# Kernel tuning notes

Measured on AMD Instinct MI355X. Metric: run time of the kernel, lower is better.

The kernel has to match this reference:

```python
import jax, jax.numpy as jnp
import numpy as np

B, A, T, D, H, NB, OUT = 64, 128, 6, 256, 512, 5, 401
ALPHA = 0.5
BETA = 0.5


def _lin_init(key, n_in, n_out, extra=()):
    bound = 1.0 / np.sqrt(n_in)
    kw, kb = jax.random.split(key)
    W = jax.random.uniform(kw, extra + (n_in, n_out), minval=-bound, maxval=bound, dtype=jnp.float32)
    b = jax.random.uniform(kb, extra + (n_out,), minval=-bound, maxval=bound, dtype=jnp.float32)
    return W, b


def setup_inputs() -> dict:
    key = jax.random.key(0)
    ks = jax.random.split(key, 8)
    stdv = 1.0 / np.sqrt(D)
    anchor = jax.random.uniform(ks[0], (1, 1, T, D), minval=-stdv, maxval=stdv, dtype=jnp.float32)
    sW1, sb1 = _lin_init(ks[1], D, D, (NB,))
    sW2, sb2 = _lin_init(ks[2], D, D, (NB,))
    cW1, cb1 = _lin_init(ks[3], D, D, (NB,))
    cW2, cb2 = _lin_init(ks[4], D, D, (NB,))
    dW1, db1 = _lin_init(ks[5], D, H)
    dW2, db2 = _lin_init(ks[6], H, OUT)
    final_embedding = jax.random.normal(ks[7], (B, A, D), dtype=jnp.float32)
    return {"final_embedding": final_embedding, "anchor": anchor,
            "sW1": sW1, "sb1": sb1, "sW2": sW2, "sb2": sb2,
            "cW1": cW1, "cb1": cb1, "cW2": cW2, "cb2": cb2,
            "dW1": dW1, "db1": db1, "dW2": dW2, "db2": db2}


def _mlp2(x, W1, b1, W2, b2):
    # 2-layer MLP (Linear -> ReLU -> Linear), applied to last dim
    return jax.nn.relu(x @ W1 + b1) @ W2 + b2


def reference(final_embedding, anchor, sW1, sb1, sW2, sb2, cW1, cb1, cW2, cb2, dW1, db1, dW2, db2):
    b, a = final_embedding.shape[:2]
    # s: [B, A, T, D] repeated anchors; c: [B, A, 1, D] context
    s = jnp.broadcast_to(anchor, (b, a, T, D))
    c = final_embedding[:, :, None, :]
    for i in range(NB):
        s_new = _mlp2(s, sW1[i], sb1[i], sW2[i], sb2[i])
        c_new = _mlp2(c, cW1[i], cb1[i], cW2[i], cb2[i])
        s_new = s_new * c_new                      # gate, broadcasts over T
        agg_c = jnp.max(s_new, axis=-2, keepdims=True)
        s = ALPHA * s + BETA * s_new               # sliding running mean
        c = ALPHA * c + BETA * agg_c
    # decoder MLP on trajectory embeddings s: [B, A, T, D]
    res = jax.nn.relu(s @ dW1 + db1) @ dW2 + db2   # [B, A, T, 401]
    coordinates = res[..., :160].reshape(b, a, T, 80, 2)
    av = res[..., 160:240].reshape(b, a, T, 80, 1)
    bv = res[..., 240:320].reshape(b, a, T, 80, 1)
    cv = res[..., 320:400].reshape(b, a, T, 80, 1)
    probas = res[..., -1]                          # [B, A, T]
    cov = jnp.concatenate([jnp.exp(av) * jnp.cosh(bv), jnp.sinh(bv),
                           jnp.sinh(bv), jnp.exp(-av) * jnp.cosh(bv)], axis=-1) * jnp.exp(cv)
    covariance_matrices = cov.reshape(b, a, T, 80, 2, 2)
    return (probas, coordinates, covariance_matrices)
```

## Files before the change

kernel.cpp:

```cpp
#include <hip/hip_runtime.h>
#include <math.h>


constexpr int Tn  = 6;
constexpr int Dn  = 256;
constexpr int Hn  = 512;
constexpr int NBn = 5;
constexpr int OUTn = 401;
constexpr int BA  = 8192;
constexpr int MR  = 49152;
constexpr float kAlpha = 0.5f;
constexpr float kBeta  = 0.5f;

typedef __bf16 bf16_8 __attribute__((ext_vector_type(8)));
typedef float  f32x4  __attribute__((ext_vector_type(4)));

__device__ __forceinline__ void async_copy16(const __bf16* g, __bf16* l) {
  __builtin_amdgcn_global_load_lds(
      (const __attribute__((address_space(1))) void*)g,
      (__attribute__((address_space(3))) void*)l, 16, 0, 0);
}

template<bool RELU, bool OUT_BF16>
__global__ __launch_bounds__(256) void gemm_mfma(
    const __bf16* __restrict__ A, const __bf16* __restrict__ BT,
    const float* __restrict__ bias, void* __restrict__ Cout,
    int M, int N, int K)
{
  __shared__ __align__(16) char smem[34816];

  const int tid = threadIdx.x;
  const int l   = tid & 63;
  const int w   = tid >> 6;
  const int wm  = w >> 1, wn = w & 1;

  const int GX = gridDim.x;
  const int total = GX * gridDim.y;
  const int L = blockIdx.y * GX + blockIdx.x;
  const int xcd = L & 7, pos = L >> 3;
  const int base = total >> 3, rem = total & 7;
  const int start = xcd * base + (xcd < rem ? xcd : rem);
  const int TL = start + pos;
  const int my = TL / GX;
  const int nx = TL - my * GX;
  const int m0 = my * 128;
  const int n0 = nx * 128;

  const int lrow = l >> 2;
  const int lk   = (l & 3) * 8;
  int ar0 = m0 + w * 32 + lrow;        if (ar0 > M - 1) ar0 = M - 1;
  int ar1 = m0 + w * 32 + 16 + lrow;   if (ar1 > M - 1) ar1 = M - 1;
  int br0 = n0 + w * 32 + lrow;        if (br0 > N - 1) br0 = N - 1;
  int br1 = n0 + w * 32 + 16 + lrow;   if (br1 > N - 1) br1 = N - 1;
  const __bf16* Ag0 = A  + (size_t)ar0 * K + lk;
  const __bf16* Ag1 = A  + (size_t)ar1 * K + lk;
  const __bf16* Bg0 = BT + (size_t)br0 * K + lk;
  const __bf16* Bg1 = BT + (size_t)br1 * K + lk;

  f32x4 acc[4][4];
#pragma unroll
  for (int i = 0; i < 4; ++i)
#pragma unroll
    for (int j = 0; j < 4; ++j) acc[i][j] = (f32x4){0.f, 0.f, 0.f, 0.f};

  auto stage = [&](int buf, int ko) {
    __bf16* As = (__bf16*)(smem + buf * 16384);
    __bf16* Bs = As + 4096;
    async_copy16(Ag0 + ko, As + w * 1024);
    async_copy16(Ag1 + ko, As + w * 1024 + 512);
    async_copy16(Bg0 + ko, Bs + w * 1024);
    async_copy16(Bg1 + ko, Bs + w * 1024 + 512);
  };

  const int kIters = K >> 5;
  stage(0, 0);
  __syncthreads();
  for (int kt = 0; kt < kIters; ++kt) {
    if (kt + 1 < kIters) stage((kt + 1) & 1, (kt + 1) * 32);
    const __bf16* As = (const __bf16*)(smem + (kt & 1) * 16384);
    const __bf16* Bs = As + 4096;
    const __bf16* ap = As + (wm * 64 + (l & 15)) * 32 + (l >> 4) * 8;
    const __bf16* bp = Bs + (wn * 64 + (l & 15)) * 32 + (l >> 4) * 8;

    bf16_8 af[4], bf[4];
#pragma unroll
    for (int i = 0; i < 4; ++i) af[i] = *(const bf16_8*)(ap + i * 16 * 32);
#pragma unroll
    for (int j = 0; j < 4; ++j) bf[j] = *(const bf16_8*)(bp + j * 16 * 32);
#pragma unroll
    for (int i = 0; i < 4; ++i)
#pragma unroll
      for (int j = 0; j < 4; ++j)
        acc[i][j] = __builtin_amdgcn_mfma_f32_16x16x32_bf16(af[i], bf[j], acc[i][j], 0, 0, 0);
    __syncthreads();
  }

  const int colb = n0 + wn * 64 + (l & 15);
  const int rowb = m0 + wm * 64 + (l >> 4) * 4;

  if (OUT_BF16) {
    __bf16* Cs = (__bf16*)smem;
    const int lrb = wm * 64 + (l >> 4) * 4;
    const int lcb = wn * 64 + (l & 15);
#pragma unroll
    for (int j = 0; j < 4; ++j) {
      const float bj = bias[colb + j * 16];
#pragma unroll
      for (int i = 0; i < 4; ++i) {
#pragma unroll
        for (int r = 0; r < 4; ++r) {
          float v = acc[i][j][r] + bj;
          if (RELU) v = fmaxf(v, 0.0f);
          Cs[(lrb + i * 16 + r) * 136 + lcb + j * 16] = (__bf16)v;
        }
      }
    }
    __syncthreads();
    __bf16* Cg = (__bf16*)Cout;
#pragma unroll
    for (int it = 0; it < 8; ++it) {
      const int idx = it * 256 + tid;
      const int row = idx >> 4, c16 = idx & 15;
      const int gr = m0 + row;
      if (gr < M) {
        uint4 v = *(const uint4*)(Cs + row * 136 + c16 * 8);
        *(uint4*)(Cg + (size_t)gr * N + n0 + c16 * 8) = v;
      }
    }
  } else {
#pragma unroll
    for (int j = 0; j < 4; ++j) {
      const int gc = colb + j * 16;
      if (gc >= N) continue;
      const float bj = bias[gc];
#pragma unroll
      for (int i = 0; i < 4; ++i) {
        const int gr0 = rowb + i * 16;
#pragma unroll
        for (int r = 0; r < 4; ++r) {
          const int gr = gr0 + r;
          if (gr >= M) continue;
          float v = acc[i][j][r] + bj;
          if (RELU) v = fmaxf(v, 0.0f);
          ((float*)Cout)[(size_t)gr * N + gc] = v;
        }
      }
    }
  }
}

__global__ __launch_bounds__(512) void mlp2_c(
    const __bf16* __restrict__ X, const __bf16* __restrict__ W1T,
    const float* __restrict__ b1, const __bf16* __restrict__ W2T,
    const float* __restrict__ b2, __bf16* __restrict__ Out)
{
  __shared__ __align__(16) char smem[53248];
  __bf16* Hb = (__bf16*)(smem + 36864);

  const int tid = threadIdx.x, l = tid & 63, w = tid >> 6;
  const int m0 = blockIdx.x * 32;
  const int q4 = (l >> 4) * 4;

  f32x4 acc[2][2];
#pragma unroll
  for (int i = 0; i < 2; ++i)
#pragma unroll
    for (int j = 0; j < 2; ++j) acc[i][j] = (f32x4){0.f, 0.f, 0.f, 0.f};

  const __bf16* Xg = X + (size_t)(m0 + (tid >> 2)) * Dn + (tid & 3) * 8;

  auto stageA = [&](int buf, int kt) {
    if (tid < 128)
      async_copy16(Xg + kt * 32, (__bf16*)(smem + buf * 2048) + tid * 8);
  };
  auto stageW = [&](const __bf16* WT, int buf, int kt) {
    __bf16* Wstb = (__bf16*)(smem + 4096 + buf * 16384);
#pragma unroll
    for (int r2 = 0; r2 < 2; ++r2) {
      const int ch = tid + r2 * 512, row = ch >> 2, kk = (ch & 3) * 8;
      async_copy16(WT + (size_t)row * Dn + kt * 32 + kk, Wstb + ch * 8);
    }
  };

  stageA(0, 0); stageW(W1T, 0, 0);
  __syncthreads();
  for (int kt = 0; kt < 8; ++kt) {
    if (kt < 7) { stageA((kt + 1) & 1, kt + 1); stageW(W1T, (kt + 1) & 1, kt + 1); }
    const __bf16* Astb = (const __bf16*)(smem + (kt & 1) * 2048);
    const __bf16* Wstb = (const __bf16*)(smem + 4096 + (kt & 1) * 16384);
    bf16_8 bf[2];
#pragma unroll
    for (int j = 0; j < 2; ++j)
      bf[j] = *(const bf16_8*)(Wstb + (w * 32 + j * 16 + (l & 15)) * 32 + (l >> 4) * 8);
#pragma unroll
    for (int i = 0; i < 2; ++i) {
      bf16_8 af = *(const bf16_8*)(Astb + (i * 16 + (l & 15)) * 32 + (l >> 4) * 8);
#pragma unroll
      for (int j = 0; j < 2; ++j)
        acc[i][j] = __builtin_amdgcn_mfma_f32_16x16x32_bf16(af, bf[j], acc[i][j], 0, 0, 0);
    }
    __syncthreads();
  }

#pragma unroll
  for (int j = 0; j < 2; ++j) {
    const int col = w * 32 + j * 16 + (l & 15);
    const float bj = b1[col];
    __bf16* hc = Hb + (col >> 5) * 1024 + (col & 31);
#pragma unroll
    for (int i = 0; i < 2; ++i)
#pragma unroll
      for (int r = 0; r < 4; ++r) {
        const int row = i * 16 + q4 + r;
        hc[row * 32] = (__bf16)fmaxf(acc[i][j][r] + bj, 0.0f);
      }
  }
  __syncthreads();

#pragma unroll
  for (int i = 0; i < 2; ++i)
#pragma unroll
    for (int j = 0; j < 2; ++j) acc[i][j] = (f32x4){0.f, 0.f, 0.f, 0.f};
  stageW(W2T, 0, 0);
  __syncthreads();
  for (int kt = 0; kt < 8; ++kt) {
    if (kt < 7) stageW(W2T, (kt + 1) & 1, kt + 1);
    const __bf16* Wstb = (const __bf16*)(smem + 4096 + (kt & 1) * 16384);
    bf16_8 bf[2];
#pragma unroll
    for (int j = 0; j < 2; ++j)
      bf[j] = *(const bf16_8*)(Wstb + (w * 32 + j * 16 + (l & 15)) * 32 + (l >> 4) * 8);
#pragma unroll
    for (int i = 0; i < 2; ++i) {
      bf16_8 af = *(const bf16_8*)(Hb + kt * 1024 + (i * 16 + (l & 15)) * 32 + (l >> 4) * 8);
#pragma unroll
      for (int j = 0; j < 2; ++j)
        acc[i][j] = __builtin_amdgcn_mfma_f32_16x16x32_bf16(af, bf[j], acc[i][j], 0, 0, 0);
    }
    __syncthreads();
  }

#pragma unroll
  for (int j = 0; j < 2; ++j) {
    const int col = w * 32 + j * 16 + (l & 15);
    const float bj = b2[col];
#pragma unroll
    for (int i = 0; i < 2; ++i)
#pragma unroll
      for (int r = 0; r < 4; ++r) {
        const int row = i * 16 + q4 + r;
        Out[(size_t)(m0 + row) * Dn + col] = (__bf16)(acc[i][j][r] + bj);
      }
  }
}

__global__ __launch_bounds__(512) void mlp2_cs(
    __bf16* __restrict__ S,
    const __bf16* __restrict__ sW1T, const float* __restrict__ sb1,
    const __bf16* __restrict__ sW2T, const float* __restrict__ sb2,
    const __bf16* __restrict__ cW1T, const float* __restrict__ cb1,
    const __bf16* __restrict__ cW2T, const float* __restrict__ cb2,
    __bf16* __restrict__ C)
{
  __shared__ __align__(16) char smem[71680];
  __bf16* Hb    = (__bf16*)(smem + 22528);
  __bf16* Snew  = (__bf16*)smem;
  __bf16* Hc    = (__bf16*)(smem + 45056);
  __bf16* CnewL = (__bf16*)(smem + 53248);

  const int tid = threadIdx.x, l = tid & 63, w = tid >> 6;
  const int m0  = blockIdx.x * 96;
  const int ba0 = blockIdx.x * 16;
  const int q4  = (l >> 4) * 4;

  {
    f32x4 ac[2];
    ac[0] = (f32x4){0.f, 0.f, 0.f, 0.f};
    ac[1] = (f32x4){0.f, 0.f, 0.f, 0.f};

    const __bf16* Cg = C + (size_t)(ba0 + (tid >> 2)) * Dn + (tid & 3) * 8;

    auto stageC1 = [&](int buf, int kt) {
      __bf16* Astb = (__bf16*)(smem + buf * 22528);
      __bf16* Wstb = Astb + 3072;
      if (tid < 64) async_copy16(Cg + kt * 32, Astb + tid * 8);
#pragma unroll
      for (int r2 = 0; r2 < 2; ++r2) {
        const int ch = tid + r2 * 512, row = ch >> 2, kk = (ch & 3) * 8;
        async_copy16(cW1T + (size_t)row * Dn + kt * 32 + kk, Wstb + ch * 8);
      }
    };
    stageC1(0, 0);
    __syncthreads();
    for (int kt = 0; kt < 8; ++kt) {
      if (kt < 7) stageC1((kt + 1) & 1, kt + 1);
      const __bf16* Astb = (const __bf16*)(smem + (kt & 1) * 22528);
      const __bf16* Wstb = Astb + 3072;
      bf16_8 bf[2];
#pragma unroll
      for (int j = 0; j < 2; ++j)
        bf[j] = *(const bf16_8*)(Wstb + (w * 32 + j * 16 + (l & 15)) * 32 + (l >> 4) * 8);
      bf16_8 af = *(const bf16_8*)(Astb + (l & 15) * 32 + (l >> 4) * 8);
#pragma unroll
      for (int j = 0; j < 2; ++j)
        ac[j] = __builtin_amdgcn_mfma_f32_16x16x32_bf16(af, bf[j], ac[j], 0, 0, 0);
      __syncthreads();
    }

#pragma unroll
    for (int j = 0; j < 2; ++j) {
      const int col = w * 32 + j * 16 + (l & 15);
      const float bj = cb1[col];
      __bf16* hc = Hc + (col >> 5) * 512 + (col & 31);
#pragma unroll
      for (int r = 0; r < 4; ++r)
        hc[(q4 + r) * 32] = (__bf16)fmaxf(ac[j][r] + bj, 0.0f);
    }
    __syncthreads();

    ac[0] = (f32x4){0.f, 0.f, 0.f, 0.f};
    ac[1] = (f32x4){0.f, 0.f, 0.f, 0.f};
    auto stageC2 = [&](int buf, int kt) {
      __bf16* Wstb = (__bf16*)(smem + buf * 22528 + 6144);
#pragma unroll
      for (int r2 = 0; r2 < 2; ++r2) {
        const int ch = tid + r2 * 512, row = ch >> 2, kk = (ch & 3) * 8;
        async_copy16(cW2T + (size_t)row * Dn + kt * 32 + kk, Wstb + ch * 8);
      }
    };
    stageC2(0, 0);
    __syncthreads();
    for (int kt = 0; kt < 8; ++kt) {
      if (kt < 7) stageC2((kt + 1) & 1, kt + 1);
      const __bf16* Wstb = (const __bf16*)(smem + (kt & 1) * 22528 + 6144);
      bf16_8 bf[2];
#pragma unroll
      for (int j = 0; j < 2; ++j)
        bf[j] = *(const bf16_8*)(Wstb + (w * 32 + j * 16 + (l & 15)) * 32 + (l >> 4) * 8);
      bf16_8 af = *(const bf16_8*)(Hc + kt * 512 + (l & 15) * 32 + (l >> 4) * 8);
#pragma unroll
      for (int j = 0; j < 2; ++j)
        ac[j] = __builtin_amdgcn_mfma_f32_16x16x32_bf16(af, bf[j], ac[j], 0, 0, 0);
      __syncthreads();
    }

#pragma unroll
    for (int j = 0; j < 2; ++j) {
      const int col = w * 32 + j * 16 + (l & 15);
      const float bj = cb2[col];
#pragma unroll
      for (int r = 0; r < 4; ++r)
        CnewL[(q4 + r) * 264 + col] = (__bf16)(ac[j][r] + bj);
    }
    __syncthreads();
  }

  bf16_8 cn8 = *(const bf16_8*)(CnewL + (tid >> 5) * 264 + (tid & 31) * 8);

  f32x4 acc[6][2];
#pragma unroll
  for (int i = 0; i < 6; ++i)
#pragma unroll
    for (int j = 0; j < 2; ++j) acc[i][j] = (f32x4){0.f, 0.f, 0.f, 0.f};

  const __bf16* Sg = S + (size_t)(m0 + (tid >> 2)) * Dn + (tid & 3) * 8;

  auto stageL1 = [&](int buf, int kt) {
    __bf16* Astb = (__bf16*)(smem + buf * 22528);
    __bf16* Wstb = (__bf16*)(smem + buf * 22528 + 6144);
    if (tid < 384) async_copy16(Sg + kt * 32, Astb + tid * 8);
#pragma unroll
    for (int r2 = 0; r2 < 2; ++r2) {
      const int ch = tid + r2 * 512, row = ch >> 2, kk = (ch & 3) * 8;
      async_copy16(sW1T + (size_t)row * Dn + kt * 32 + kk, Wstb + ch * 8);
    }
  };

  stageL1(0, 0);
  __syncthreads();
  for (int kt = 0; kt < 8; ++kt) {
    if (kt < 7) stageL1((kt + 1) & 1, kt + 1);
    const __bf16* Astb = (const __bf16*)(smem + (kt & 1) * 22528);
    const __bf16* Wstb = Astb + 3072;
    bf16_8 bf[2];
#pragma unroll
    for (int j = 0; j < 2; ++j)
      bf[j] = *(const bf16_8*)(Wstb + (w * 32 + j * 16 + (l & 15)) * 32 + (l >> 4) * 8);
#pragma unroll
    for (int i = 0; i < 6; ++i) {
      bf16_8 af = *(const bf16_8*)(Astb + (i * 16 + (l & 15)) * 32 + (l >> 4) * 8);
#pragma unroll
      for (int j = 0; j < 2; ++j)
        acc[i][j] = __builtin_amdgcn_mfma_f32_16x16x32_bf16(af, bf[j], acc[i][j], 0, 0, 0);
    }
    __syncthreads();
  }

#pragma unroll
  for (int j = 0; j < 2; ++j) {
    const int col = w * 32 + j * 16 + (l & 15);
    const float bj = sb1[col];
    __bf16* hc = Hb + (col >> 5) * (96 * 32) + (col & 31);
#pragma unroll
    for (int i = 0; i < 6; ++i)
#pragma unroll
      for (int r = 0; r < 4; ++r) {
        const int row = i * 16 + q4 + r;
        hc[row * 32] = (__bf16)fmaxf(acc[i][j][r] + bj, 0.0f);
      }
  }
  __syncthreads();

#pragma unroll
  for (int i = 0; i < 6; ++i)
#pragma unroll
    for (int j = 0; j < 2; ++j) acc[i][j] = (f32x4){0.f, 0.f, 0.f, 0.f};
  __bf16* Wst = (__bf16*)(smem + 6144);
  for (int kt = 0; kt < 8; ++kt) {
#pragma unroll
    for (int r2 = 0; r2 < 2; ++r2) {
      const int ch = tid + r2 * 512, row = ch >> 2, kk = (ch & 3) * 8;
      async_copy16(sW2T + (size_t)row * Dn + kt * 32 + kk, Wst + ch * 8);
    }
    __syncthreads();
    bf16_8 bf[2];
#pragma unroll
    for (int j = 0; j < 2; ++j)
      bf[j] = *(const bf16_8*)(Wst + (w * 32 + j * 16 + (l & 15)) * 32 + (l >> 4) * 8);
#pragma unroll
    for (int i = 0; i < 6; ++i) {
      bf16_8 af = *(const bf16_8*)(Hb + kt * (96 * 32) + (i * 16 + (l & 15)) * 32 + (l >> 4) * 8);
#pragma unroll
      for (int j = 0; j < 2; ++j)
        acc[i][j] = __builtin_amdgcn_mfma_f32_16x16x32_bf16(af, bf[j], acc[i][j], 0, 0, 0);
    }
    __syncthreads();
  }

#pragma unroll
  for (int j = 0; j < 2; ++j) {
    const int col = w * 32 + j * 16 + (l & 15);
    const float bj = sb2[col];
#pragma unroll
    for (int i = 0; i < 6; ++i)
#pragma unroll
      for (int r = 0; r < 4; ++r) {
        const int row = i * 16 + q4 + r;
        Snew[row * 264 + col] = (__bf16)(acc[i][j][r] + bj);
      }
  }
  __syncthreads();

  {
    const int ba = tid >> 5, dg = (tid & 31) * 8;
    const size_t gb = (size_t)(ba0 + ba) * Dn + dg;
    float cn[8], m[8];
#pragma unroll
    for (int e = 0; e < 8; ++e) { cn[e] = (float)cn8[e]; m[e] = -3.402823466e38f; }
#pragma unroll
    for (int t = 0; t < Tn; ++t) {
      const int row = ba * 6 + t;
      bf16_8 sn8 = *(const bf16_8*)(Snew + row * 264 + dg);
      const size_t gs = (size_t)(m0 + row) * Dn + dg;
      bf16_8 s8 = *(const bf16_8*)(S + gs);
      bf16_8 o8;
#pragma unroll
      for (int e = 0; e < 8; ++e) {
        const float sn = (float)sn8[e] * cn[e];
        m[e] = fmaxf(m[e], sn);
        o8[e] = (__bf16)(kAlpha * (float)s8[e] + kBeta * sn);
      }
      *(bf16_8*)(S + gs) = o8;
    }
    bf16_8 c8 = *(const bf16_8*)(C + gb);
#pragma unroll
    for (int e = 0; e < 8; ++e)
      c8[e] = (__bf16)(kAlpha * (float)c8[e] + kBeta * m[e]);
    *(bf16_8*)(C + gb) = c8;
  }
}

__global__ __launch_bounds__(512, 4) void decoder_fused(
    const __bf16* __restrict__ S, const __bf16* __restrict__ W1T,
    const float* __restrict__ b1, const __bf16* __restrict__ W2T,
    const float* __restrict__ bias, float* __restrict__ out)
{
  __shared__ __align__(16) char smem[49152];
  __bf16* Ast = (__bf16*)smem;
  __bf16* W1s = (__bf16*)(smem + 32768);
  __bf16* Hb  = (__bf16*)(smem + 40960);
  float*  mid = (float*)smem;

  const int tid = threadIdx.x, l = tid & 63, w = tid >> 6;
  const int m0 = blockIdx.x * 64;
  const int q4 = (l >> 4) * 4;
  const int rt  = w >> 1;
  const int ch2 = (w & 1) * 32;

  f32x4 acc[4][4];
#pragma unroll
  for (int i = 0; i < 4; ++i)
#pragma unroll
    for (int j = 0; j < 4; ++j) acc[i][j] = (f32x4){0.f, 0.f, 0.f, 0.f};

  if (tid < 256) {
    const __bf16* Sg = S + (size_t)(m0 + (tid >> 2)) * Dn + (tid & 3) * 8;
#pragma unroll
    for (int kt = 0; kt < 8; ++kt)
      async_copy16(Sg + kt * 32, Ast + kt * 2048 + tid * 8);
  }

  const __bf16* W2p[4];
#pragma unroll
  for (int j = 0; j < 4; ++j) {
    int col = w * 64 + j * 16 + (l & 15);
    if (col > 400) col = 400;
    W2p[j] = W2T + (size_t)col * Hn + (l >> 4) * 8;
  }

  const int wkk = (tid & 3) * 8;

  for (int cc = 0; cc < 8; ++cc) {
    if (tid < 256)
      async_copy16(W1T + (size_t)(cc * 64 + (tid >> 2)) * Dn + wkk,
                   W1s + tid * 8);
    __syncthreads();

    f32x4 a1[2];
    a1[0] = (f32x4){0.f, 0.f, 0.f, 0.f};
    a1[1] = (f32x4){0.f, 0.f, 0.f, 0.f};
    for (int kt = 0; kt < 8; ++kt) {
      if (kt < 7 && tid < 256)
        async_copy16(W1T + (size_t)(cc * 64 + (tid >> 2)) * Dn + (kt + 1) * 32 + wkk,
                     W1s + ((kt + 1) & 1) * 2048 + tid * 8);
      const __bf16* Wb = W1s + (kt & 1) * 2048;
      bf16_8 af = *(const bf16_8*)(Ast + kt * 2048 + (rt * 16 + (l & 15)) * 32 + (l >> 4) * 8);
#pragma unroll
      for (int j = 0; j < 2; ++j) {
        bf16_8 bw = *(const bf16_8*)(Wb + (ch2 + j * 16 + (l & 15)) * 32 + (l >> 4) * 8);
        a1[j] = __builtin_amdgcn_mfma_f32_16x16x32_bf16(af, bw, a1[j], 0, 0, 0);
      }
      __syncthreads();
    }

#pragma unroll
    for (int j = 0; j < 2; ++j) {
      const int col = ch2 + j * 16 + (l & 15);
      const float bj = b1[cc * 64 + col];
      __bf16* hp = Hb + (col >> 5) * 2048 + (col & 31);
#pragma unroll
      for (int r = 0; r < 4; ++r)
        hp[(rt * 16 + q4 + r) * 32] = (__bf16)fmaxf(a1[j][r] + bj, 0.0f);
    }
    __syncthreads();

#pragma unroll
    for (int kt2 = 0; kt2 < 2; ++kt2) {
      bf16_8 af2[4], bf2[4];
#pragma unroll
      for (int j = 0; j < 4; ++j)
        bf2[j] = *(const bf16_8*)(W2p[j] + cc * 64 + kt2 * 32);
#pragma unroll
      for (int i = 0; i < 4; ++i)
        af2[i] = *(const bf16_8*)(Hb + kt2 * 2048 + (i * 16 + (l & 15)) * 32 + (l >> 4) * 8);
#pragma unroll
      for (int i = 0; i < 4; ++i)
#pragma unroll
        for (int j = 0; j < 4; ++j)
          acc[i][j] = __builtin_amdgcn_mfma_f32_16x16x32_bf16(af2[i], bf2[j], acc[i][j], 0, 0, 0);
    }
    __syncthreads();
  }

  float* cov = out + MR + (size_t)MR * 160;
  const int gc = w * 64 + (l & 15);
#pragma unroll
  for (int sub = 0; sub < 2; ++sub) {
#pragma unroll
    for (int ih = 0; ih < 2; ++ih) {
      const int i = sub * 2 + ih;
#pragma unroll
      for (int j = 0; j < 4; ++j) {
        const int c = gc + j * 16;
        if (c > 400) continue;
        const float bj = bias[c];
#pragma unroll
        for (int r = 0; r < 4; ++r) {
          const int lr = ih * 16 + q4 + r;
          const int gr = m0 + sub * 32 + lr;
          const float v = acc[i][j][r] + bj;
          if (c < 160)      out[(size_t)MR + (size_t)gr * 160 + c] = v;
          else if (c < 400) mid[lr * 241 + (c - 160)] = v;
          else              out[gr] = v;
        }
      }
    }
    __syncthreads();
#pragma unroll
    for (int p = 0; p < 5; ++p) {
      const int q = p * 512 + tid;
      const int r32 = q / 80, j = q - r32 * 80;
      const int gr = m0 + sub * 32 + r32;
      const float av = mid[r32 * 241 + j];
      const float bv = mid[r32 * 241 + 80 + j];
      const float cv = mid[r32 * 241 + 160 + j];
      const float eb = __expf(bv), ebn = __expf(-bv);
      const float sh = 0.5f * (eb - ebn), ch = 0.5f * (eb + ebn);
      const float ea = __expf(av), ean = __expf(-av), ec = __expf(cv);
      f32x4 c4 = { ea * ch * ec, sh * ec, sh * ec, ean * ch * ec };
      *(f32x4*)(cov + (size_t)gr * 320 + 4 * j) = c4;
    }
    if (sub == 0) __syncthreads();
  }
}

__global__ __launch_bounds__(256) void transpose_bf16(
    const float* __restrict__ W, __bf16* __restrict__ WT, int K, int N)
{
  __shared__ float t[32][33];
  const int b  = blockIdx.z;
  const int tx = threadIdx.x, ty = threadIdx.y;
  const int k0 = blockIdx.y * 32, n0 = blockIdx.x * 32;
  const float* Wb  = W  + (size_t)b * K * N;
  __bf16*      WTb = WT + (size_t)b * N * K;
#pragma unroll
  for (int r = 0; r < 4; ++r) {
    int kk = k0 + ty + r * 8;
    if (kk < K && n0 + tx < N) t[ty + r * 8][tx] = Wb[(size_t)kk * N + n0 + tx];
  }
  __syncthreads();
#pragma unroll
  for (int r = 0; r < 4; ++r) {
    int nn = n0 + ty + r * 8;
    if (nn < N && k0 + tx < K)
      WTb[(size_t)nn * K + k0 + tx] = (__bf16)t[tx][ty + r * 8];
  }
}

__global__ __launch_bounds__(256) void convert_bf16(
    const float* __restrict__ in, __bf16* __restrict__ out, int n)
{
  int i = blockIdx.x * 256 + threadIdx.x;
  if (i < n) out[i] = (__bf16)in[i];
}

__global__ __launch_bounds__(256) void ew_update0(
    const float* __restrict__ anchor, const float* __restrict__ fe,
    const float* __restrict__ snewsm, const __bf16* __restrict__ cnew,
    __bf16* __restrict__ s, __bf16* __restrict__ c)
{
  int q = blockIdx.x * 256 + threadIdx.x;
  if (q >= BA * 32) return;
  int ba = q >> 5;
  int dg = (q & 31) * 8;
  bf16_8 cn8 = *(const bf16_8*)(cnew + (size_t)ba * Dn + dg);
  float cn[8], m[8];
#pragma unroll
  for (int e = 0; e < 8; ++e) { cn[e] = (float)cn8[e]; m[e] = -3.402823466e38f; }
  size_t base = (size_t)ba * Tn * Dn + dg;
#pragma unroll
  for (int t = 0; t < Tn; ++t) {
    bf16_8 o8;
#pragma unroll
    for (int e = 0; e < 8; ++e) {
      float sn = snewsm[t * Dn + dg + e] * cn[e];
      m[e] = fmaxf(m[e], sn);
      o8[e] = (__bf16)(kAlpha * anchor[t * Dn + dg + e] + kBeta * sn);
    }
    *(bf16_8*)(s + base + t * Dn) = o8;
  }
  bf16_8 c8;
#pragma unroll
  for (int e = 0; e < 8; ++e)
    c8[e] = (__bf16)(kAlpha * fe[(size_t)ba * Dn + dg + e] + kBeta * m[e]);
  *(bf16_8*)(c + (size_t)ba * Dn + dg) = c8;
}

extern "C" void kernel_launch(void* const* d_in, const int* in_sizes, int n_in,
                              void* d_out, int out_size, void* d_ws, size_t ws_size,
                              hipStream_t stream) {
  const float* fe     = (const float*)d_in[0];
  const float* anchor = (const float*)d_in[1];
  const float* sW1 = (const float*)d_in[2];
  const float* sb1 = (const float*)d_in[3];
  const float* sW2 = (const float*)d_in[4];
  const float* sb2 = (const float*)d_in[5];
  const float* cW1 = (const float*)d_in[6];
  const float* cb1 = (const float*)d_in[7];
  const float* cW2 = (const float*)d_in[8];
  const float* cb2 = (const float*)d_in[9];
  const float* dW1 = (const float*)d_in[10];
  const float* db1 = (const float*)d_in[11];
  const float* dW2 = (const float*)d_in[12];
  const float* db2 = (const float*)d_in[13];
  float* out = (float*)d_out;

  char* p = (char*)d_ws;
  __bf16* s_bf    = (__bf16*)(p + 0);
  __bf16* c_bf    = (__bf16*)(p + 75497472);
  __bf16* cnew_bf = (__bf16*)(p + 79691776);
  __bf16* fe_bf   = (__bf16*)(p + 83886080);
  __bf16* sWT1    = (__bf16*)(p + 88080384);
  __bf16* sWT2    = (__bf16*)(p + 88735744);
  __bf16* cWT1    = (__bf16*)(p + 89391104);
  __bf16* cWT2    = (__bf16*)(p + 90046464);
  __bf16* dWT1    = (__bf16*)(p + 90701824);
  __bf16* dWT2    = (__bf16*)(p + 90963968);
  __bf16* anc_bf  = (__bf16*)(p + 91374592);
  __bf16* hsm_bf  = (__bf16*)(p + 91377664);
  float*  snewsm_f= (float* )(p + 91380736);

  auto gemm = [&](const __bf16* A, const __bf16* BT, const float* b, void* C,
                  int M, int N, int K, bool relu, bool outbf) {
    dim3 grid((N + 127) / 128, (M + 127) / 128);
    if (relu) {
      if (outbf) gemm_mfma<true,  true ><<<grid, 256, 0, stream>>>(A, BT, b, C, M, N, K);
      else       gemm_mfma<true,  false><<<grid, 256, 0, stream>>>(A, BT, b, C, M, N, K);
    } else {
      if (outbf) gemm_mfma<false, true ><<<grid, 256, 0, stream>>>(A, BT, b, C, M, N, K);
      else       gemm_mfma<false, false><<<grid, 256, 0, stream>>>(A, BT, b, C, M, N, K);
    }
  };

  {
    dim3 blk(32, 8);
    dim3 g88(8, 8, NBn);
    transpose_bf16<<<g88, blk, 0, stream>>>(sW1, sWT1, Dn, Dn);
    transpose_bf16<<<g88, blk, 0, stream>>>(sW2, sWT2, Dn, Dn);
    transpose_bf16<<<g88, blk, 0, stream>>>(cW1, cWT1, Dn, Dn);
    transpose_bf16<<<g88, blk, 0, stream>>>(cW2, cWT2, Dn, Dn);
    transpose_bf16<<<dim3(16, 8, 1), blk, 0, stream>>>(dW1, dWT1, Dn, Hn);
    transpose_bf16<<<dim3(13, 16, 1), blk, 0, stream>>>(dW2, dWT2, Hn, OUTn);
  }
  convert_bf16<<<(BA * Dn + 255) / 256, 256, 0, stream>>>(fe, fe_bf, BA * Dn);
  convert_bf16<<<(Tn * Dn + 255) / 256, 256, 0, stream>>>(anchor, anc_bf, Tn * Dn);

  const size_t WKK = (size_t)Dn * Dn;

  gemm(anc_bf, sWT1, sb1, hsm_bf,   Tn, Dn, Dn, true,  true);
  gemm(hsm_bf, sWT2, sb2, snewsm_f, Tn, Dn, Dn, false, false);
  mlp2_c<<<BA / 32, 512, 0, stream>>>(fe_bf, cWT1, cb1, cWT2, cb2, cnew_bf);
  ew_update0<<<(BA * 32 + 255) / 256, 256, 0, stream>>>(anchor, fe, snewsm_f,
                                                        cnew_bf, s_bf, c_bf);

  for (int i = 1; i < NBn; ++i) {
    mlp2_cs<<<MR / 96, 512, 0, stream>>>(
        s_bf,
        sWT1 + i * WKK, sb1 + i * Dn, sWT2 + i * WKK, sb2 + i * Dn,
        cWT1 + i * WKK, cb1 + i * Dn, cWT2 + i * WKK, cb2 + i * Dn,
        c_bf);
  }

  decoder_fused<<<MR / 64, 512, 0, stream>>>(s_bf, dWT1, db1, dWT2, db2, out);
}
```

Before: 387.0 us.

## Stage full W1 chunk per block and overlap its load with GEMM2

After: 378.2 us. 1.02x faster.

```diff
diff --git a/kernel.cpp b/kernel.cpp
--- a/kernel.cpp
+++ b/kernel.cpp
@@ -485,10 +485,10 @@
     const float* __restrict__ b1, const __bf16* __restrict__ W2T,
     const float* __restrict__ bias, float* __restrict__ out)
 {
-  __shared__ __align__(16) char smem[49152];
+  __shared__ __align__(16) char smem[73728];
   __bf16* Ast = (__bf16*)smem;
   __bf16* W1s = (__bf16*)(smem + 32768);
-  __bf16* Hb  = (__bf16*)(smem + 40960);
+  __bf16* Hb  = (__bf16*)(smem + 65536);
   float*  mid = (float*)smem;
 
   const int tid = threadIdx.x, l = tid & 63, w = tid >> 6;
@@ -503,12 +503,21 @@
 #pragma unroll
     for (int j = 0; j < 4; ++j) acc[i][j] = (f32x4){0.f, 0.f, 0.f, 0.f};
 
-  if (tid < 256) {
-    const __bf16* Sg = S + (size_t)(m0 + (tid >> 2)) * Dn + (tid & 3) * 8;
-#pragma unroll
-    for (int kt = 0; kt < 8; ++kt)
-      async_copy16(Sg + kt * 32, Ast + kt * 2048 + tid * 8);
-  }
+#pragma unroll
+  for (int r4 = 0; r4 < 4; ++r4) {
+    const int q = tid + r4 * 512;
+    const int ktq = q >> 8, row = (q >> 2) & 63, kk = (q & 3) * 8;
+    async_copy16(S + (size_t)(m0 + row) * Dn + ktq * 32 + kk, Ast + q * 8);
+  }
+
+  auto stageW1 = [&](int cc) {
+#pragma unroll
+    for (int r4 = 0; r4 < 4; ++r4) {
+      const int q = tid + r4 * 512;
+      const int ktq = q >> 8, row = (q >> 2) & 63, kk = (q & 3) * 8;
+      async_copy16(W1T + (size_t)(cc * 64 + row) * Dn + ktq * 32 + kk, W1s + q * 8);
+    }
+  };
 
   const __bf16* W2p[4];
 #pragma unroll
@@ -518,29 +527,21 @@
     W2p[j] = W2T + (size_t)col * Hn + (l >> 4) * 8;
   }
 
-  const int wkk = (tid & 3) * 8;
+  stageW1(0);
+  __syncthreads();
 
   for (int cc = 0; cc < 8; ++cc) {
-    if (tid < 256)
-      async_copy16(W1T + (size_t)(cc * 64 + (tid >> 2)) * Dn + wkk,
-                   W1s + tid * 8);
-    __syncthreads();
-
     f32x4 a1[2];
     a1[0] = (f32x4){0.f, 0.f, 0.f, 0.f};
     a1[1] = (f32x4){0.f, 0.f, 0.f, 0.f};
+#pragma unroll
     for (int kt = 0; kt < 8; ++kt) {
-      if (kt < 7 && tid < 256)
-        async_copy16(W1T + (size_t)(cc * 64 + (tid >> 2)) * Dn + (kt + 1) * 32 + wkk,
-                     W1s + ((kt + 1) & 1) * 2048 + tid * 8);
-      const __bf16* Wb = W1s + (kt & 1) * 2048;
       bf16_8 af = *(const bf16_8*)(Ast + kt * 2048 + (rt * 16 + (l & 15)) * 32 + (l >> 4) * 8);
 #pragma unroll
       for (int j = 0; j < 2; ++j) {
-        bf16_8 bw = *(const bf16_8*)(Wb + (ch2 + j * 16 + (l & 15)) * 32 + (l >> 4) * 8);
+        bf16_8 bw = *(const bf16_8*)(W1s + kt * 2048 + (ch2 + j * 16 + (l & 15)) * 32 + (l >> 4) * 8);
         a1[j] = __builtin_amdgcn_mfma_f32_16x16x32_bf16(af, bw, a1[j], 0, 0, 0);
       }
-      __syncthreads();
     }
 
 #pragma unroll
@@ -553,6 +554,8 @@
         hp[(rt * 16 + q4 + r) * 32] = (__bf16)fmaxf(a1[j][r] + bj, 0.0f);
     }
     __syncthreads();
+
+    if (cc < 7) stageW1(cc + 1);
 
 #pragma unroll
     for (int kt2 = 0; kt2 < 2; ++kt2) {
```
